# Kernel tuning notes

Measured on AMD Instinct MI355X. Metric: run time of the kernel, lower is better.

## Reference

```python
import jax, jax.numpy as jnp
import numpy as np

KQ_D = 64  # head dim from init_kwargs

def setup_inputs() -> dict:
    key = jax.random.key(0)
    k1, k2, k3, k4 = jax.random.split(key, 4)
    B, H, S, D = 2, 12, 2048, KQ_D
    q = jax.random.normal(k1, (B, H, S, D), dtype=jnp.float32)
    k = jax.random.normal(k2, (B, H, S, D), dtype=jnp.float32)
    v = jax.random.normal(k3, (B, H, S, D), dtype=jnp.float32)
    mask = jax.random.randint(k4, (B, 1, S, S), 0, 2, dtype=jnp.int32)
    return {"q": q, "k": k, "v": v, "mask": mask}

def reference(q, k, v, mask):
    # attn = (q @ k^T) / sqrt(kq_d)
    scale = 1.0 / (KQ_D ** 0.5)
    attn = jnp.einsum('bhqd,bhkd->bhqk', q, k) * scale
    # masked_fill(mask == 0, -1e9)
    attn = jnp.where(mask == 0, jnp.float32(-1e9), attn)
    # softmax over keys; dropout is identity in eval/reference mode
    attn = jax.nn.softmax(attn, axis=-1)
    out = jnp.einsum('bhqk,bhkd->bhqd', attn, v)
    return out
```

## Files before the change

kernel.cpp:

```cpp
#include <hip/hip_runtime.h>
#include <hip/hip_bf16.h>

#define S_LEN 2048
#define D_DIM 64
#define NH    12
#define NB    2
#define BH_N  (NB*NH)
#define TILES 32
#define TILE_BYTES 16384
#define KV_WS_BYTES ((size_t)BH_N * TILES * TILE_BYTES)
#define MASK_WORDS  ((size_t)NB * S_LEN * TILES)
#define WS_NEEDED   (KV_WS_BYTES + MASK_WORDS * 8)

typedef __attribute__((ext_vector_type(8))) short short8;
typedef __attribute__((ext_vector_type(4))) float f32x4;

static __device__ inline unsigned bfbits(float f) {
    __hip_bfloat16 h = __float2bfloat16(f);
    return (unsigned)*reinterpret_cast<const unsigned short*>(&h);
}

static __device__ inline void gload_lds16(const void* g, unsigned ldsoff) {
    __builtin_amdgcn_global_load_lds(
        (__attribute__((address_space(1))) void*)(unsigned long long)(uintptr_t)g,
        (__attribute__((address_space(3))) void*)(unsigned long long)ldsoff,
        16, 0, 0);
}

__global__ __launch_bounds__(256) void prep(const float* __restrict__ k,
                                            const float* __restrict__ v,
                                            const int* __restrict__ mask,
                                            char* __restrict__ wsKV,
                                            unsigned long long* __restrict__ wm) {
    __shared__ __align__(16) float sv[64 * 68];
    const int tid = threadIdx.x;
    const int bid = blockIdx.x;
    if (bid < 768) {
        const int t = bid & 31, bh = bid >> 5;
        const int kv0 = t * 64;
        const float* kb = k + (size_t)bh * (S_LEN * D_DIM);
        const float* vb = v + (size_t)bh * (S_LEN * D_DIM);
        char* img = wsKV + ((size_t)bh * TILES + t) * TILE_BYTES;

#pragma unroll
        for (int g = 0; g < 4; ++g) {
            int i = g * 256 + tid;
            int row = i >> 4, cb = (i & 15) << 3;
            int cp = cb ^ ((row & 7) << 4);
            float4 f = *(const float4*)(kb + (size_t)(kv0 + row) * D_DIM + (cp >> 1));
            uint2 u;
            u.x = bfbits(f.x) | (bfbits(f.y) << 16);
            u.y = bfbits(f.z) | (bfbits(f.w) << 16);
            *(uint2*)(img + (size_t)i * 8) = u;
            float4 fv = *(const float4*)(vb + (size_t)(kv0 + row) * D_DIM + ((i & 15) << 2));
            *(float4*)&sv[row * 68 + ((i & 15) << 2)] = fv;
        }
        __syncthreads();
#pragma unroll
        for (int g = 0; g < 4; ++g) {
            int i = g * 256 + tid;
            int drow = i >> 4, cb = (i & 15) << 3;
            int cp = cb ^ ((drow & 7) << 4);
            int key0 = cp >> 1;
            uint2 u;
            u.x = bfbits(sv[(key0 + 0) * 68 + drow]) | (bfbits(sv[(key0 + 1) * 68 + drow]) << 16);
            u.y = bfbits(sv[(key0 + 2) * 68 + drow]) | (bfbits(sv[(key0 + 3) * 68 + drow]) << 16);
            *(uint2*)(img + 8192 + (size_t)i * 8) = u;
        }
    } else {
        const int lane = tid & 63;
        const int wgid = (bid - 768) * 4 + (tid >> 6);
#pragma unroll 1
        for (int g = 0; g < 16; ++g) {
            const int t0 = wgid * 64 + g * 4;
            const size_t base = (size_t)t0 * 64 + lane;
            int m0 = mask[base];
            int m1 = mask[base + 64];
            int m2 = mask[base + 128];
            int m3 = mask[base + 192];
            unsigned long long b0 = __ballot(m0 != 0);
            unsigned long long b1 = __ballot(m1 != 0);
            unsigned long long b2 = __ballot(m2 != 0);
            unsigned long long b3 = __ballot(m3 != 0);
            if (lane == 0) {
                wm[t0 + 0] = b0; wm[t0 + 1] = b1;
                wm[t0 + 2] = b2; wm[t0 + 3] = b3;
            }
        }
    }
}

__global__ __launch_bounds__(256, 3) void attn_main(
    const float* __restrict__ q, const char* __restrict__ wsKV,
    const unsigned long long* __restrict__ wm, float* __restrict__ out)
{
    __shared__ __align__(16) char smem[2 * TILE_BYTES + 8192];

    const int tid  = threadIdx.x;
    const int wave = tid >> 6;
    const int lane = tid & 63;
    const int l16  = lane & 15;
    const int lhi  = lane >> 4;

    const int f  = blockIdx.x;
    const int n  = (f & 7) * 96 + (f >> 3);
    const int bx = n & 31;
    const int bh = n >> 5;
    const int b  = bh / NH;
    const int qw = bx * 64 + wave * 16;
    const int qq = qw + l16;

    const float* qb = q + (size_t)bh * (S_LEN * D_DIM);
    float*       ob = out + (size_t)bh * (S_LEN * D_DIM);
    const char*  tileBase = wsKV + (size_t)bh * TILES * TILE_BYTES;
    const size_t widx = ((size_t)b * S_LEN + qq) * TILES;

    const float PRE = 0.125f * 1.44269504088896f;

    short8 bq[2];
#pragma unroll
    for (int ks = 0; ks < 2; ++ks) {
        const float* src = qb + (size_t)qq * D_DIM + ks * 32 + lhi * 8;
        float4 f0 = *(const float4*)(src);
        float4 f1 = *(const float4*)(src + 4);
        short8 a;
        a[0] = (short)bfbits(f0.x * PRE); a[1] = (short)bfbits(f0.y * PRE);
        a[2] = (short)bfbits(f0.z * PRE); a[3] = (short)bfbits(f0.w * PRE);
        a[4] = (short)bfbits(f1.x * PRE); a[5] = (short)bfbits(f1.y * PRE);
        a[6] = (short)bfbits(f1.z * PRE); a[7] = (short)bfbits(f1.w * PRE);
        bq[ks] = a;
    }

    f32x4 o[4];
#pragma unroll
    for (int dt = 0; dt < 4; ++dt) o[dt] = (f32x4){0.f, 0.f, 0.f, 0.f};
    float mrun = -1e30f, lrun = 0.f;

    const unsigned smem_base = (unsigned)(uintptr_t)(&smem[0]);
    char* pw = smem + 2 * TILE_BYTES + wave * 2048;

    unsigned long long mw = wm[widx];
#pragma unroll
    for (int j = 0; j < 4; ++j) {
        unsigned off = (unsigned)(wave * 4096 + j * 1024 + lane * 16);
        gload_lds16(tileBase + off, smem_base + off);
    }
    __syncthreads();

    int buf = 0;
    for (int t = 0; t < 32; ++t) {
        if (t < 31) {
            const char* timg = tileBase + (size_t)(t + 1) * TILE_BYTES;
            unsigned dstb = smem_base + (unsigned)((buf ^ 1) * TILE_BYTES);
#pragma unroll
            for (int j = 0; j < 4; ++j) {
                unsigned off = (unsigned)(wave * 4096 + j * 1024 + lane * 16);
                gload_lds16(timg + off, dstb + off);
            }
        }
        unsigned long long mw_next = (t < 31) ? wm[widx + t + 1] : 0ull;

        const char* sK  = smem + buf * TILE_BYTES;
        const char* sVt = sK + 8192;

        f32x4 sc[4];
#pragma unroll
        for (int tt = 0; tt < 4; ++tt) sc[tt] = (f32x4){0.f, 0.f, 0.f, 0.f};
#pragma unroll
        for (int ks = 0; ks < 2; ++ks) {
#pragma unroll
            for (int tt = 0; tt < 4; ++tt) {
                int row = tt * 16 + l16;
                int byte = row * 128 + ((ks * 64 + lhi * 16) ^ ((row & 7) << 4));
                short8 ak = *(const short8*)(sK + byte);
                sc[tt] = __builtin_amdgcn_mfma_f32_16x16x32_bf16(ak, bq[ks], sc[tt], 0, 0, 0);
            }
        }

        short8 bvv[2][4];
#pragma unroll
        for (int ks = 0; ks < 2; ++ks)
#pragma unroll
            for (int dt = 0; dt < 4; ++dt) {
                int drow = dt * 16 + l16;
                int vbyte = drow * 128 + ((ks * 64 + lhi * 16) ^ ((drow & 7) << 4));
                bvv[ks][dt] = *(const short8*)(sVt + vbyte);
            }

        float pm = -1e30f;
#pragma unroll
        for (int tt = 0; tt < 4; ++tt) {
            unsigned nib = (unsigned)(mw >> (tt * 16 + lhi * 4)) & 0xFu;
#pragma unroll
            for (int r = 0; r < 4; ++r) {
                float s = ((nib >> r) & 1u) ? sc[tt][r] : -1e9f;
                sc[tt][r] = s;
                pm = fmaxf(pm, s);
            }
        }
        pm = fmaxf(pm, __shfl_xor(pm, 16));
        pm = fmaxf(pm, __shfl_xor(pm, 32));

        if (!__all(pm - mrun <= 8.0f)) {
            float mnew = fmaxf(mrun, pm);
            float fsc = exp2f(mrun - mnew);
            mrun = mnew;
            lrun *= fsc;
            float fr[4];
#pragma unroll
            for (int r = 0; r < 4; ++r) fr[r] = __shfl(fsc, lhi * 4 + r);
#pragma unroll
            for (int dt = 0; dt < 4; ++dt)
#pragma unroll
                for (int r = 0; r < 4; ++r) o[dt][r] *= fr[r];
        }

        float rs = 0.f;
#pragma unroll
        for (int tt = 0; tt < 4; ++tt)
#pragma unroll
            for (int r = 0; r < 4; ++r) {
                float p = exp2f(sc[tt][r] - mrun);
                sc[tt][r] = p;
                rs += p;
            }

#pragma unroll
        for (int tt = 0; tt < 4; ++tt) {
            uint2 u;
            u.x = bfbits(sc[tt][0]) | (bfbits(sc[tt][1]) << 16);
            u.y = bfbits(sc[tt][2]) | (bfbits(sc[tt][3]) << 16);
            int byte = l16 * 128 + (((tt * 16 + lhi * 4) * 2) ^ ((l16 & 7) << 4));
            *(uint2*)(pw + byte) = u;
        }

        rs += __shfl_xor(rs, 16);
        rs += __shfl_xor(rs, 32);
        lrun += rs;

#pragma unroll
        for (int ks = 0; ks < 2; ++ks) {
            int pbyte = l16 * 128 + ((ks * 64 + lhi * 16) ^ ((l16 & 7) << 4));
            short8 pa = *(const short8*)(pw + pbyte);
#pragma unroll
            for (int dt = 0; dt < 4; ++dt)
                o[dt] = __builtin_amdgcn_mfma_f32_16x16x32_bf16(pa, bvv[ks][dt], o[dt], 0, 0, 0);
        }

        __syncthreads();
        buf ^= 1;
        mw = mw_next;
    }

    float invl = 1.0f / lrun;
    float ir[4];
#pragma unroll
    for (int r = 0; r < 4; ++r) ir[r] = __shfl(invl, lhi * 4 + r);
#pragma unroll
    for (int dt = 0; dt < 4; ++dt)
#pragma unroll
        for (int r = 0; r < 4; ++r) {
            int qrow = qw + lhi * 4 + r;
            int dcol = dt * 16 + l16;
            ob[(size_t)qrow * D_DIM + dcol] = o[dt][r] * ir[r];
        }
}

__global__ __launch_bounds__(256, 3) void attn_fallback(
    const float* __restrict__ q, const float* __restrict__ k,
    const float* __restrict__ v, const int* __restrict__ mask,
    float* __restrict__ out)
{
    __shared__ __align__(16) unsigned short sK[4096];
    __shared__ __align__(16) unsigned short sVt[4096];
    __shared__ __align__(16) unsigned short sP[4096];

    const int tid  = threadIdx.x;
    const int wave = tid >> 6;
    const int lane = tid & 63;
    const int l16  = lane & 15;
    const int lhi  = lane >> 4;

    const int bh = blockIdx.y;
    const int b  = bh / NH;
    const int q0 = blockIdx.x * 64;
    const int qw = q0 + wave * 16;
    const int qq = qw + l16;

    const float* qbase = q + (size_t)bh * S_LEN * D_DIM;
    const float* kbase = k + (size_t)bh * S_LEN * D_DIM;
    const float* vbase = v + (size_t)bh * S_LEN * D_DIM;
    const int*   mp = mask + (size_t)b * S_LEN * S_LEN + (size_t)qq * S_LEN;

    const float PRE = 0.125f * 1.44269504088896f;

    short8 bq[2];
#pragma unroll
    for (int ks = 0; ks < 2; ++ks) {
        const float* src = qbase + (size_t)qq * D_DIM + ks * 32 + lhi * 8;
        float4 f0 = *(const float4*)(src);
        float4 f1 = *(const float4*)(src + 4);
        short8 a;
        a[0] = (short)bfbits(f0.x * PRE); a[1] = (short)bfbits(f0.y * PRE);
        a[2] = (short)bfbits(f0.z * PRE); a[3] = (short)bfbits(f0.w * PRE);
        a[4] = (short)bfbits(f1.x * PRE); a[5] = (short)bfbits(f1.y * PRE);
        a[6] = (short)bfbits(f1.z * PRE); a[7] = (short)bfbits(f1.w * PRE);
        bq[ks] = a;
    }

    f32x4 o[4];
#pragma unroll
    for (int dt = 0; dt < 4; ++dt) o[dt] = (f32x4){0.f, 0.f, 0.f, 0.f};
    float mrun = -1e30f, lrun = 0.f;
    unsigned short* pw = sP + wave * 1024;

    int srow[4], sd[4];
#pragma unroll
    for (int s = 0; s < 4; ++s) { int i = tid + 256 * s; srow[s] = i >> 4; sd[s] = (i & 15) * 4; }

    float4 kreg[4], vreg[4];
#pragma unroll
    for (int s = 0; s < 4; ++s) {
        kreg[s] = *(const float4*)(kbase + (size_t)srow[s] * D_DIM + sd[s]);
        vreg[s] = *(const float4*)(vbase + (size_t)srow[s] * D_DIM + sd[s]);
    }

    for (int kv0 = 0; kv0 < S_LEN; kv0 += 64) {
        __syncthreads();
#pragma unroll
        for (int s = 0; s < 4; ++s) {
            unsigned p0 = bfbits(kreg[s].x) | (bfbits(kreg[s].y) << 16);
            unsigned p1 = bfbits(kreg[s].z) | (bfbits(kreg[s].w) << 16);
            int byte = srow[s] * 128 + ((sd[s] * 2) ^ ((srow[s] & 7) << 4));
            *(uint2*)((char*)sK + byte) = make_uint2(p0, p1);
        }
#pragma unroll
        for (int s = 0; s < 4; ++s) {
            float ff[4] = {vreg[s].x, vreg[s].y, vreg[s].z, vreg[s].w};
#pragma unroll
            for (int jj = 0; jj < 4; ++jj) {
                int dd = sd[s] + jj;
                int byte = dd * 128 + ((srow[s] * 2) ^ ((dd & 7) << 4));
                *(unsigned short*)((char*)sVt + byte) = (unsigned short)bfbits(ff[jj]);
            }
        }
        __syncthreads();

        if (kv0 + 64 < S_LEN) {
#pragma unroll
            for (int s = 0; s < 4; ++s) {
                kreg[s] = *(const float4*)(kbase + (size_t)(kv0 + 64 + srow[s]) * D_DIM + sd[s]);
                vreg[s] = *(const float4*)(vbase + (size_t)(kv0 + 64 + srow[s]) * D_DIM + sd[s]);
            }
        }

        int4 m0 = *(const int4*)(mp + kv0 + lhi * 4);
        int4 m1 = *(const int4*)(mp + kv0 + 16 + lhi * 4);
        int4 m2 = *(const int4*)(mp + kv0 + 32 + lhi * 4);
        int4 m3 = *(const int4*)(mp + kv0 + 48 + lhi * 4);

        f32x4 sc[4];
#pragma unroll
        for (int tt = 0; tt < 4; ++tt) sc[tt] = (f32x4){0.f, 0.f, 0.f, 0.f};
#pragma unroll
        for (int ks = 0; ks < 2; ++ks) {
#pragma unroll
            for (int tt = 0; tt < 4; ++tt) {
                int row = tt * 16 + l16;
                int byte = row * 128 + ((ks * 64 + lhi * 16) ^ ((row & 7) << 4));
                short8 ak = *(const short8*)((const char*)sK + byte);
                sc[tt] = __builtin_amdgcn_mfma_f32_16x16x32_bf16(ak, bq[ks], sc[tt], 0, 0, 0);
            }
        }

        const int4 mm[4] = {m0, m1, m2, m3};
        float pm = -1e30f;
#pragma unroll
        for (int tt = 0; tt < 4; ++tt)
#pragma unroll
            for (int r = 0; r < 4; ++r) {
                float s = ((const int*)&mm[tt])[r] ? sc[tt][r] : -1e9f;
                sc[tt][r] = s;
                pm = fmaxf(pm, s);
            }
        pm = fmaxf(pm, __shfl_xor(pm, 16));
        pm = fmaxf(pm, __shfl_xor(pm, 32));

        float mnew = fmaxf(mrun, pm);
        float fsc = exp2f(mrun - mnew);
        mrun = mnew;
        float rs = 0.f;
#pragma unroll
        for (int tt = 0; tt < 4; ++tt)
#pragma unroll
            for (int r = 0; r < 4; ++r) {
                float p = exp2f(sc[tt][r] - mnew);
                sc[tt][r] = p;
                rs += p;
            }
        rs += __shfl_xor(rs, 16);
        rs += __shfl_xor(rs, 32);
        lrun = lrun * fsc + rs;

        float fr[4];
#pragma unroll
        for (int r = 0; r < 4; ++r) fr[r] = __shfl(fsc, lhi * 4 + r);
#pragma unroll
        for (int dt = 0; dt < 4; ++dt)
#pragma unroll
            for (int r = 0; r < 4; ++r) o[dt][r] *= fr[r];

#pragma unroll
        for (int tt = 0; tt < 4; ++tt) {
            unsigned p0 = bfbits(sc[tt][0]) | (bfbits(sc[tt][1]) << 16);
            unsigned p1 = bfbits(sc[tt][2]) | (bfbits(sc[tt][3]) << 16);
            int byte = l16 * 128 + (((tt * 16 + lhi * 4) * 2) ^ ((l16 & 7) << 4));
            *(uint2*)((char*)pw + byte) = make_uint2(p0, p1);
        }

#pragma unroll
        for (int ks = 0; ks < 2; ++ks) {
            int pbyte = l16 * 128 + ((ks * 64 + lhi * 16) ^ ((l16 & 7) << 4));
            short8 pa = *(const short8*)((const char*)pw + pbyte);
#pragma unroll
            for (int dt = 0; dt < 4; ++dt) {
                int drow = dt * 16 + l16;
                int vbyte = drow * 128 + ((ks * 64 + lhi * 16) ^ ((drow & 7) << 4));
                short8 bv = *(const short8*)((const char*)sVt + vbyte);
                o[dt] = __builtin_amdgcn_mfma_f32_16x16x32_bf16(pa, bv, o[dt], 0, 0, 0);
            }
        }
    }

    float invl = 1.0f / lrun;
    float ir[4];
#pragma unroll
    for (int r = 0; r < 4; ++r) ir[r] = __shfl(invl, lhi * 4 + r);
#pragma unroll
    for (int dt = 0; dt < 4; ++dt)
#pragma unroll
        for (int r = 0; r < 4; ++r) {
            int qrow = qw + lhi * 4 + r;
            int dcol = dt * 16 + l16;
            out[(size_t)bh * S_LEN * D_DIM + (size_t)qrow * D_DIM + dcol] = o[dt][r] * ir[r];
        }
}

extern "C" void kernel_launch(void* const* d_in, const int* in_sizes, int n_in,
                              void* d_out, int out_size, void* d_ws, size_t ws_size,
                              hipStream_t stream) {
    const float* q   = (const float*)d_in[0];
    const float* k   = (const float*)d_in[1];
    const float* v   = (const float*)d_in[2];
    const int* mask  = (const int*)d_in[3];
    float* out = (float*)d_out;

    if (ws_size >= WS_NEEDED) {
        char* ws = (char*)d_ws;
        char* wsKV = ws;
        unsigned long long* wm = (unsigned long long*)(ws + KV_WS_BYTES);
        prep<<<dim3(1280), dim3(256), 0, stream>>>(k, v, mask, wsKV, wm);
        attn_main<<<dim3(768), dim3(256), 0, stream>>>(q, wsKV, wm, out);
    } else {
        attn_fallback<<<dim3(S_LEN / 64, BH_N), dim3(256), 0, stream>>>(q, k, v, mask, out);
    }
}
```

Baseline: 84.12 us.

## Load V tiles straight into registers, stage only K through LDS

The preprocessing kernel now writes the transposed V image in a layout that matches the MFMA B-operand lane order, without swizzle. The main loop loads V for the next tile straight from global memory into registers, double-buffered through two register sets in a manually unrolled pair of tile bodies. Only K is staged through LDS via global_load_lds, which halves LDS per block. This removes the LDS round-trip and LDS reads for V and may allow higher occupancy, at the cost of more VGPRs and exposed global-load latency.

```diff
diff --git a/kernel.cpp b/kernel.cpp
--- a/kernel.cpp
+++ b/kernel.cpp
@@ -59,9 +59,8 @@
 #pragma unroll
         for (int g = 0; g < 4; ++g) {
             int i = g * 256 + tid;
-            int drow = i >> 4, cb = (i & 15) << 3;
-            int cp = cb ^ ((drow & 7) << 4);
-            int key0 = cp >> 1;
+            int drow = i >> 4;
+            int key0 = (i & 15) * 4;
             uint2 u;
             u.x = bfbits(sv[(key0 + 0) * 68 + drow]) | (bfbits(sv[(key0 + 1) * 68 + drow]) << 16);
             u.y = bfbits(sv[(key0 + 2) * 68 + drow]) | (bfbits(sv[(key0 + 3) * 68 + drow]) << 16);
@@ -94,7 +93,7 @@
     const float* __restrict__ q, const char* __restrict__ wsKV,
     const unsigned long long* __restrict__ wm, float* __restrict__ out)
 {
-    __shared__ __align__(16) char smem[2 * TILE_BYTES + 8192];
+    __shared__ __align__(16) char smem[2 * 8192 + 8192];
 
     const int tid  = threadIdx.x;
     const int wave = tid >> 6;
@@ -137,120 +136,134 @@
     float mrun = -1e30f, lrun = 0.f;
 
     const unsigned smem_base = (unsigned)(uintptr_t)(&smem[0]);
-    char* pw = smem + 2 * TILE_BYTES + wave * 2048;
+    char* pw = smem + 16384 + wave * 2048;
+    const int laneoff = l16 * 128 + lhi * 16;
+
+    short8 va0, va1, va2, va3, va4, va5, va6, va7;
+    short8 vb0, vb1, vb2, vb3, vb4, vb5, vb6, vb7;
 
     unsigned long long mw = wm[widx];
-#pragma unroll
-    for (int j = 0; j < 4; ++j) {
-        unsigned off = (unsigned)(wave * 4096 + j * 1024 + lane * 16);
-        gload_lds16(tileBase + off, smem_base + off);
+    unsigned long long mwn;
+
+    gload_lds16(tileBase + tid * 16, smem_base + tid * 16);
+    gload_lds16(tileBase + 4096 + tid * 16, smem_base + 4096 + tid * 16);
+    {
+        const char* vimg = tileBase + 8192 + laneoff;
+        va0 = *(const short8*)(vimg + 0 * 2048 + 0 * 64);
+        va1 = *(const short8*)(vimg + 0 * 2048 + 1 * 64);
+        va2 = *(const short8*)(vimg + 1 * 2048 + 0 * 64);
+        va3 = *(const short8*)(vimg + 1 * 2048 + 1 * 64);
+        va4 = *(const short8*)(vimg + 2 * 2048 + 0 * 64);
+        va5 = *(const short8*)(vimg + 2 * 2048 + 1 * 64);
+        va6 = *(const short8*)(vimg + 3 * 2048 + 0 * 64);
+        va7 = *(const short8*)(vimg + 3 * 2048 + 1 * 64);
     }
     __syncthreads();
 
-    int buf = 0;
-    for (int t = 0; t < 32; ++t) {
-        if (t < 31) {
-            const char* timg = tileBase + (size_t)(t + 1) * TILE_BYTES;
-            unsigned dstb = smem_base + (unsigned)((buf ^ 1) * TILE_BYTES);
-#pragma unroll
-            for (int j = 0; j < 4; ++j) {
-                unsigned off = (unsigned)(wave * 4096 + j * 1024 + lane * 16);
-                gload_lds16(timg + off, dstb + off);
-            }
-        }
-        unsigned long long mw_next = (t < 31) ? wm[widx + t + 1] : 0ull;
-
-        const char* sK  = smem + buf * TILE_BYTES;
-        const char* sVt = sK + 8192;
-
-        f32x4 sc[4];
-#pragma unroll
-        for (int tt = 0; tt < 4; ++tt) sc[tt] = (f32x4){0.f, 0.f, 0.f, 0.f};
-#pragma unroll
-        for (int ks = 0; ks < 2; ++ks) {
-#pragma unroll
-            for (int tt = 0; tt < 4; ++tt) {
-                int row = tt * 16 + l16;
-                int byte = row * 128 + ((ks * 64 + lhi * 16) ^ ((row & 7) << 4));
-                short8 ak = *(const short8*)(sK + byte);
-                sc[tt] = __builtin_amdgcn_mfma_f32_16x16x32_bf16(ak, bq[ks], sc[tt], 0, 0, 0);
-            }
-        }
-
-        short8 bvv[2][4];
-#pragma unroll
-        for (int ks = 0; ks < 2; ++ks)
-#pragma unroll
-            for (int dt = 0; dt < 4; ++dt) {
-                int drow = dt * 16 + l16;
-                int vbyte = drow * 128 + ((ks * 64 + lhi * 16) ^ ((drow & 7) << 4));
-                bvv[ks][dt] = *(const short8*)(sVt + vbyte);
-            }
-
-        float pm = -1e30f;
-#pragma unroll
-        for (int tt = 0; tt < 4; ++tt) {
-            unsigned nib = (unsigned)(mw >> (tt * 16 + lhi * 4)) & 0xFu;
-#pragma unroll
-            for (int r = 0; r < 4; ++r) {
-                float s = ((nib >> r) & 1u) ? sc[tt][r] : -1e9f;
-                sc[tt][r] = s;
-                pm = fmaxf(pm, s);
-            }
-        }
-        pm = fmaxf(pm, __shfl_xor(pm, 16));
-        pm = fmaxf(pm, __shfl_xor(pm, 32));
-
-        if (!__all(pm - mrun <= 8.0f)) {
-            float mnew = fmaxf(mrun, pm);
-            float fsc = exp2f(mrun - mnew);
-            mrun = mnew;
-            lrun *= fsc;
-            float fr[4];
-#pragma unroll
-            for (int r = 0; r < 4; ++r) fr[r] = __shfl(fsc, lhi * 4 + r);
-#pragma unroll
-            for (int dt = 0; dt < 4; ++dt)
-#pragma unroll
-                for (int r = 0; r < 4; ++r) o[dt][r] *= fr[r];
-        }
-
-        float rs = 0.f;
-#pragma unroll
-        for (int tt = 0; tt < 4; ++tt)
-#pragma unroll
-            for (int r = 0; r < 4; ++r) {
-                float p = exp2f(sc[tt][r] - mrun);
-                sc[tt][r] = p;
-                rs += p;
-            }
-
-#pragma unroll
-        for (int tt = 0; tt < 4; ++tt) {
-            uint2 u;
-            u.x = bfbits(sc[tt][0]) | (bfbits(sc[tt][1]) << 16);
-            u.y = bfbits(sc[tt][2]) | (bfbits(sc[tt][3]) << 16);
-            int byte = l16 * 128 + (((tt * 16 + lhi * 4) * 2) ^ ((l16 & 7) << 4));
-            *(uint2*)(pw + byte) = u;
-        }
-
-        rs += __shfl_xor(rs, 16);
-        rs += __shfl_xor(rs, 32);
-        lrun += rs;
-
-#pragma unroll
-        for (int ks = 0; ks < 2; ++ks) {
-            int pbyte = l16 * 128 + ((ks * 64 + lhi * 16) ^ ((l16 & 7) << 4));
-            short8 pa = *(const short8*)(pw + pbyte);
-#pragma unroll
-            for (int dt = 0; dt < 4; ++dt)
-                o[dt] = __builtin_amdgcn_mfma_f32_16x16x32_bf16(pa, bvv[ks][dt], o[dt], 0, 0, 0);
-        }
-
-        __syncthreads();
-        buf ^= 1;
-        mw = mw_next;
-    }
+#define TILE_BODY(T, V0, V1, V2, V3, V4, V5, V6, V7, N0, N1, N2, N3, N4, N5, N6, N7, RBUF, WBUF) \
+    {                                                                                             \
+        const int t_ = (T);                                                                       \
+        if (t_ < 31) {                                                                            \
+            const char* timg = tileBase + (size_t)(t_ + 1) * TILE_BYTES;                          \
+            unsigned dstb = smem_base + (WBUF) * 8192;                                            \
+            gload_lds16(timg + tid * 16, dstb + tid * 16);                                        \
+            gload_lds16(timg + 4096 + tid * 16, dstb + 4096 + tid * 16);                          \
+            const char* vimg = timg + 8192 + laneoff;                                             \
+            N0 = *(const short8*)(vimg + 0 * 2048 + 0 * 64);                                      \
+            N1 = *(const short8*)(vimg + 0 * 2048 + 1 * 64);                                      \
+            N2 = *(const short8*)(vimg + 1 * 2048 + 0 * 64);                                      \
+            N3 = *(const short8*)(vimg + 1 * 2048 + 1 * 64);                                      \
+            N4 = *(const short8*)(vimg + 2 * 2048 + 0 * 64);                                      \
+            N5 = *(const short8*)(vimg + 2 * 2048 + 1 * 64);                                      \
+            N6 = *(const short8*)(vimg + 3 * 2048 + 0 * 64);                                      \
+            N7 = *(const short8*)(vimg + 3 * 2048 + 1 * 64);                                      \
+            mwn = wm[widx + t_ + 1];                                                              \
+        }                                                                                         \
+        const char* sK = smem + (RBUF) * 8192;                                                    \
+        f32x4 sc[4];                                                                              \
+        _Pragma("unroll")                                                                         \
+        for (int tt = 0; tt < 4; ++tt) sc[tt] = (f32x4){0.f, 0.f, 0.f, 0.f};                      \
+        _Pragma("unroll")                                                                         \
+        for (int ks = 0; ks < 2; ++ks) {                                                          \
+            _Pragma("unroll")                                                                     \
+            for (int tt = 0; tt < 4; ++tt) {                                                      \
+                int row = tt * 16 + l16;                                                          \
+                int byte = row * 128 + ((ks * 64 + lhi * 16) ^ ((row & 7) << 4));                 \
+                short8 ak = *(const short8*)(sK + byte);                                          \
+                sc[tt] = __builtin_amdgcn_mfma_f32_16x16x32_bf16(ak, bq[ks], sc[tt], 0, 0, 0);    \
+            }                                                                                     \
+        }                                                                                         \
+        float pm = -1e30f;                                                                        \
+        _Pragma("unroll")                                                                         \
+        for (int tt = 0; tt < 4; ++tt) {                                                          \
+            unsigned nib = (unsigned)(mw >> (tt * 16 + lhi * 4)) & 0xFu;                          \
+            _Pragma("unroll")                                                                     \
+            for (int r = 0; r < 4; ++r) {                                                         \
+                float s = ((nib >> r) & 1u) ? sc[tt][r] : -1e9f;                                  \
+                sc[tt][r] = s;                                                                    \
+                pm = fmaxf(pm, s);                                                                \
+            }                                                                                     \
+        }                                                                                         \
+        pm = fmaxf(pm, __shfl_xor(pm, 16));                                                       \
+        pm = fmaxf(pm, __shfl_xor(pm, 32));                                                       \
+        if (!__all(pm - mrun <= 8.0f)) {                                                          \
+            float mnew = fmaxf(mrun, pm);                                                         \
+            float fsc = exp2f(mrun - mnew);                                                       \
+            mrun = mnew;                                                                          \
+            lrun *= fsc;                                                                          \
+            float fr[4];                                                                          \
+            _Pragma("unroll")                                                                     \
+            for (int r = 0; r < 4; ++r) fr[r] = __shfl(fsc, lhi * 4 + r);                         \
+            _Pragma("unroll")                                                                     \
+            for (int dt = 0; dt < 4; ++dt)                                                        \
+                _Pragma("unroll")                                                                 \
+                for (int r = 0; r < 4; ++r) o[dt][r] *= fr[r];                                    \
+        }                                                                                         \
+        float rs = 0.f;                                                                           \
+        _Pragma("unroll")                                                                         \
+        for (int tt = 0; tt < 4; ++tt)                                                            \
+            _Pragma("unroll")                                                                     \
+            for (int r = 0; r < 4; ++r) {                                                         \
+                float p = exp2f(sc[tt][r] - mrun);                                                \
+                sc[tt][r] = p;                                                                    \
+                rs += p;                                                                          \
+            }                                                                                     \
+        _Pragma("unroll")                                                                         \
+        for (int tt = 0; tt < 4; ++tt) {                                                          \
+            uint2 u;                                                                              \
+            u.x = bfbits(sc[tt][0]) | (bfbits(sc[tt][1]) << 16);                                  \
+            u.y = bfbits(sc[tt][2]) | (bfbits(sc[tt][3]) << 16);                                  \
+            int byte = l16 * 128 + (((tt * 16 + lhi * 4) * 2) ^ ((l16 & 7) << 4));                \
+            *(uint2*)(pw + byte) = u;                                                             \
+        }                                                                                         \
+        rs += __shfl_xor(rs, 16);                                                                 \
+        rs += __shfl_xor(rs, 32);                                                                 \
+        lrun += rs;                                                                               \
+        {                                                                                         \
+            int pbyte0 = l16 * 128 + ((0 * 64 + lhi * 16) ^ ((l16 & 7) << 4));                    \
+            int pbyte1 = l16 * 128 + ((1 * 64 + lhi * 16) ^ ((l16 & 7) << 4));                    \
+            short8 pa0 = *(const short8*)(pw + pbyte0);                                           \
+            short8 pa1 = *(const short8*)(pw + pbyte1);                                           \
+            o[0] = __builtin_amdgcn_mfma_f32_16x16x32_bf16(pa0, V0, o[0], 0, 0, 0);               \
+            o[0] = __builtin_amdgcn_mfma_f32_16x16x32_bf16(pa1, V1, o[0], 0, 0, 0);               \
+            o[1] = __builtin_amdgcn_mfma_f32_16x16x32_bf16(pa0, V2, o[1], 0, 0, 0);               \
+            o[1] = __builtin_amdgcn_mfma_f32_16x16x32_bf16(pa1, V3, o[1], 0, 0, 0);               \
+            o[2] = __builtin_amdgcn_mfma_f32_16x16x32_bf16(pa0, V4, o[2], 0, 0, 0);               \
+            o[2] = __builtin_amdgcn_mfma_f32_16x16x32_bf16(pa1, V5, o[2], 0, 0, 0);               \
+            o[3] = __builtin_amdgcn_mfma_f32_16x16x32_bf16(pa0, V6, o[3], 0, 0, 0);               \
+            o[3] = __builtin_amdgcn_mfma_f32_16x16x32_bf16(pa1, V7, o[3], 0, 0, 0);               \
+        }                                                                                         \
+        __syncthreads();                                                                          \
+        mw = mwn;                                                                                 \
+    }
+
+    for (int th = 0; th < 16; ++th) {
+        TILE_BODY(2 * th,     va0, va1, va2, va3, va4, va5, va6, va7,
+                              vb0, vb1, vb2, vb3, vb4, vb5, vb6, vb7, 0, 1);
+        TILE_BODY(2 * th + 1, vb0, vb1, vb2, vb3, vb4, vb5, vb6, vb7,
+                              va0, va1, va2, va3, va4, va5, va6, va7, 1, 0);
+    }
+#undef TILE_BODY
 
     float invl = 1.0f / lrun;
     float ir[4];
```

Result: slower. 130.0 us (+54.5%).
